# Performance work log

Measured on AMD Instinct MI355X. Metric: run time of the kernel, lower is better.

## Reference

```python
import jax, jax.numpy as jnp
import numpy as np

D = 1024           # input_size
D2 = 2 * D         # hidden width of the three inner linears
OUT = 1024         # output_size
S = 8192           # tokens per example


def setup_inputs() -> dict:
    key = jax.random.key(0)
    ks = jax.random.split(key, 11)
    def lin(k, fan_in, fan_out):
        bound = 1.0 / np.sqrt(fan_in)
        kw, kb = jax.random.split(k)
        W = jax.random.uniform(kw, (fan_in, fan_out), jnp.float32, -bound, bound)
        b = jax.random.uniform(kb, (fan_out,), jnp.float32, -bound, bound)
        return W, b
    W_in, b_in = lin(ks[0], D, D2)      # reading_example_input
    W_out, b_out = lin(ks[1], D, D2)    # reading_example_output
    W_cat, b_cat = lin(ks[2], D2, D2)   # concatenated_layer_map
    W_fin, b_fin = lin(ks[3], D2, OUT)  # final_map
    return {
        "input_embedding": jax.random.normal(ks[4], (1, S, D), jnp.float32),
        "output_embedding": jax.random.normal(ks[5], (1, S, D), jnp.float32),
        "random_augmentation": jax.random.normal(ks[6], (1, S, D), jnp.float32),
        "W_in": W_in, "b_in": b_in,
        "W_out": W_out, "b_out": b_out,
        "W_cat": W_cat, "b_cat": b_cat,
        "W_fin": W_fin, "b_fin": b_fin,
    }


def reference(input_embedding, output_embedding, random_augmentation,
              W_in, b_in, W_out, b_out, W_cat, b_cat, W_fin, b_fin):
    def march(x, y):
        # x, y: [1, S, D]
        iq = jax.nn.softmax(x @ W_in + b_in, axis=-1)[0]    # [S, 2D]
        oq = jax.nn.softmax(y @ W_out + b_out, axis=-1)[0]  # [S, 2D]
        cat = jnp.concatenate((x, y), axis=-1)[0]           # [S, 2D]
        icm = jax.nn.softmax(cat @ W_cat + b_cat, axis=-1)  # [S, 2D]
        iqk = iq.T @ icm                                    # [2D, 2D]
        oqk = oq.T @ icm                                    # [2D, 2D]
        meta = jax.nn.relu(iqk @ oqk.T)                     # [2D, 2D]
        scale = jnp.sqrt(jnp.float32(icm.shape[-1]))
        res = (icm @ meta) / scale                          # [S, 2D]
        return jax.nn.relu(res @ W_fin + b_fin)             # [S, OUT]

    transformation = march(input_embedding, output_embedding)
    random_desc = march(input_embedding, random_augmentation)
    return (transformation, random_desc)
```

## Files before the change

### kernel.cpp

```cpp
#include <hip/hip_runtime.h>

#define S_TOK 8192
#define DIM   1024
#define DIM2  2048
#define OUTN  1024

typedef __bf16 bf16x8 __attribute__((ext_vector_type(8)));
typedef float  f32x4  __attribute__((ext_vector_type(4)));
typedef short  s16x8  __attribute__((ext_vector_type(8)));
typedef unsigned short u16x4 __attribute__((ext_vector_type(4)));

__device__ __forceinline__ unsigned short f2bf(float x) {
  unsigned u = __builtin_bit_cast(unsigned, x);
  u = (u + 0x7FFFu + ((u >> 16) & 1u)) >> 16;
  return (unsigned short)u;
}
__device__ __forceinline__ float bf2f(unsigned short u) {
  return __builtin_bit_cast(float, (unsigned)u << 16);
}

__device__ __forceinline__ void gld_lds16(const void* g, void* l) {
  auto* g1 = reinterpret_cast<__attribute__((address_space(1))) unsigned*>(
      (unsigned long long)g);
  auto* l3 = reinterpret_cast<__attribute__((address_space(3))) unsigned*>(
      (unsigned long long)l);
  __builtin_amdgcn_global_load_lds(g1, l3, 16, 0, 0);
}

__device__ __forceinline__ int lds_off(int idx, int k) {
  int b = (idx << 7) + (k << 1);
  b ^= ((idx ^ (idx >> 3)) & 7) << 4;
  return b;
}

struct PrepTab {
  const float* in[3]; unsigned short* out[3];
  const float* win[4]; unsigned short* wout[4]; int R[4]; int C[4];
};
__global__ __launch_bounds__(256) void prep_all(PrepTab t) {
  __shared__ unsigned short tl[64 * 64];
  const int tid = threadIdx.x;
  if (blockIdx.z < 3) {
    const float* in = t.in[blockIdx.z];
    unsigned short* out = t.out[blockIdx.z];
    int i = blockIdx.x * 256 + tid;
    float4 v = ((const float4*)in)[i];
    u16x4 o;
    o[0] = f2bf(v.x); o[1] = f2bf(v.y); o[2] = f2bf(v.z); o[3] = f2bf(v.w);
    *(u16x4*)(out + (size_t)i * 4) = o;
    return;
  }
  int x = blockIdx.x;
  if (x >= 4096) return;
  int wz = x >> 10, rem = x & 1023, bx = rem & 31, by = rem >> 5;
  const int R = t.R[wz], C = t.C[wz];
  const int r0 = by << 6, c0 = bx << 6;
  if (r0 >= R || c0 >= C) return;
  const float* in = t.win[wz];
  unsigned short* out = t.wout[wz];
#pragma unroll
  for (int i = 0; i < 2; ++i) {
    int ch = tid + (i << 8);
    int r = ch >> 3, c8 = (ch & 7) << 3;
    const float* p = in + (size_t)(r0 + r) * C + c0 + c8;
    float4 a = *(const float4*)p, b = *(const float4*)(p + 4);
    s16x8 w;
    w[0] = (short)f2bf(a.x); w[1] = (short)f2bf(a.y);
    w[2] = (short)f2bf(a.z); w[3] = (short)f2bf(a.w);
    w[4] = (short)f2bf(b.x); w[5] = (short)f2bf(b.y);
    w[6] = (short)f2bf(b.z); w[7] = (short)f2bf(b.w);
    int sw = ((r ^ (r >> 3)) & 7) << 3;
    *(s16x8*)&tl[(r << 6) + (c8 ^ sw)] = w;
  }
  __syncthreads();
#pragma unroll
  for (int i = 0; i < 2; ++i) {
    int ch = tid + (i << 8);
    int c = ch >> 3, r8 = (ch & 7) << 3;
    s16x8 w;
#pragma unroll
    for (int j = 0; j < 8; ++j) {
      int rr = r8 + j;
      w[j] = (short)tl[(rr << 6) + (c ^ (((rr ^ (rr >> 3)) & 7) << 3))];
    }
    *(s16x8*)(out + (size_t)(c0 + c) * R + r0 + r8) = w;
  }
}

struct SmTab { unsigned short* T[6]; };
__global__ __launch_bounds__(512) void softmax_cols(SmTab tab) {
  unsigned short* T = tab.T[blockIdx.y];
  const int tid = threadIdx.x;
  const int colg = tid & 63, seg = tid >> 6;
  const size_t c = ((size_t)blockIdx.x << 6) + colg;
  float m = -1e30f, s = 0.f;
  for (int n = seg; n < DIM2; n += 8) {
    float v = bf2f(T[(size_t)n * S_TOK + c]);
    float mn = fmaxf(m, v);
    s = s * __expf(m - mn) + __expf(v - mn);
    m = mn;
  }
  __shared__ float redm[512], reds[512];
  redm[tid] = m; reds[tid] = s;
  __syncthreads();
  if (seg == 0) {
    float M = m, S = s;
#pragma unroll
    for (int k = 1; k < 8; ++k) {
      float mk = redm[colg + (k << 6)], sk = reds[colg + (k << 6)];
      float mn = fmaxf(M, mk);
      S = S * __expf(M - mn) + sk * __expf(mk - mn);
      M = mn;
    }
    redm[colg] = M; reds[colg] = 1.0f / S;
  }
  __syncthreads();
  m = redm[colg];
  const float inv = reds[colg];
  for (int n = seg; n < DIM2; n += 8) {
    size_t idx = (size_t)n * S_TOK + c;
    T[idx] = f2bf(__expf(bf2f(T[idx]) - m) * inv);
  }
}

struct GPtr {
  const unsigned short* A[6];
  const unsigned short* Arow2[6];
  const unsigned short* B[6];
  const unsigned short* Bk2[6];
  const float* bias[6];
  void* C[6];
  int Ks[6];
  int ldas[6];
};
struct TPar { const unsigned short* src[2]; unsigned short* dst[2]; };

template <int BIAS_ROW, int OUT_BF16, int NZG>
__global__ __launch_bounds__(256, 3) void gemm_nt(GPtr p, TPar tp, int ldb, int ldc,
                                                  float scale, int do_relu) {
  __shared__ __align__(16) char lds[32768];
  const int z = blockIdx.z;
  const int tid  = threadIdx.x;

  if (NZG >= 0 && z >= NZG) {
    const unsigned short* src = tp.src[z - NZG];
    unsigned short* dst = tp.dst[z - NZG];
    unsigned short* tl = (unsigned short*)lds;
    const int nblk = gridDim.x * gridDim.y;
    int bid = blockIdx.y * gridDim.x + blockIdx.x;
    for (int it = bid; it < (DIM2 / 64) * (S_TOK / 64); it += nblk) {
      int tx = it & (S_TOK / 64 - 1), ty = it >> 7;
      int r0 = ty << 6, c0 = tx << 6;
#pragma unroll
      for (int i = 0; i < 2; ++i) {
        int ch = tid + (i << 8);
        int r = ch >> 3, c8 = (ch & 7) << 3;
        s16x8 w = *(const s16x8*)(src + (size_t)(r0 + r) * S_TOK + c0 + c8);
        int sw = ((r ^ (r >> 3)) & 7) << 3;
        *(s16x8*)&tl[(r << 6) + (c8 ^ sw)] = w;
      }
      __syncthreads();
#pragma unroll
      for (int i = 0; i < 2; ++i) {
        int ch = tid + (i << 8);
        int c = ch >> 3, r8 = (ch & 7) << 3;
        s16x8 w;
#pragma unroll
        for (int j = 0; j < 8; ++j) {
          int rr = r8 + j;
          w[j] = (short)tl[(rr << 6) + (c ^ (((rr ^ (rr >> 3)) & 7) << 3))];
        }
        *(s16x8*)(dst + (size_t)(c0 + c) * DIM2 + r0 + r8) = w;
      }
      __syncthreads();
    }
    return;
  }

  char* As = lds;
  char* Bs = lds + 16384;
  const int lane = tid & 63;
  const int wave = tid >> 6;
  const int wm = (wave >> 1) << 6;
  const int wn = (wave & 1) << 6;
  const int m0 = blockIdx.y << 7;
  const int n0 = blockIdx.x << 7;
  const int lda = p.ldas[z];
  const int K = p.Ks[z];

  const unsigned short* Au = p.A[z];
  const unsigned short* B  = p.B[z];
  const float* bias = p.bias[z];
  void* Cv = p.C[z];

  int srow[4], sgk[4];
#pragma unroll
  for (int i = 0; i < 4; ++i) {
    int c = (wave << 8) + (i << 6) + lane;
    int row = c >> 3, kc = c & 7;
    srow[i] = row;
    sgk[i]  = (kc ^ ((row ^ (row >> 3)) & 7)) << 3;
  }

  f32x4 acc[4][4];
#pragma unroll
  for (int i = 0; i < 4; ++i)
#pragma unroll
    for (int j = 0; j < 4; ++j) acc[i][j] = {0.f, 0.f, 0.f, 0.f};

  for (int k0 = 0; k0 < K; k0 += 64) {
#pragma unroll
    for (int i = 0; i < 4; ++i) {
      char* dA = As + (((wave << 2) + i) << 10);
      char* dB = Bs + (((wave << 2) + i) << 10);
      gld_lds16(Au + (size_t)(m0 + srow[i]) * lda + k0 + sgk[i], dA);
      gld_lds16(B  + (size_t)(n0 + srow[i]) * ldb + k0 + sgk[i], dB);
    }
    __syncthreads();
#pragma unroll
    for (int ks = 0; ks < 2; ++ks) {
      bf16x8 af[4], bfr[4];
      int kk = (ks << 5) + ((lane >> 4) << 3);
#pragma unroll
      for (int t = 0; t < 4; ++t) {
        af[t]  = *(const bf16x8*)(As + lds_off(wm + (t << 4) + (lane & 15), kk));
        bfr[t] = *(const bf16x8*)(Bs + lds_off(wn + (t << 4) + (lane & 15), kk));
      }
#pragma unroll
      for (int mt = 0; mt < 4; ++mt)
#pragma unroll
        for (int nt = 0; nt < 4; ++nt)
          acc[mt][nt] = __builtin_amdgcn_mfma_f32_16x16x32_bf16(af[mt], bfr[nt], acc[mt][nt], 0, 0, 0);
    }
    __syncthreads();
  }

  if (OUT_BF16) {
    unsigned short* ct = (unsigned short*)lds;
    __syncthreads();
#pragma unroll
    for (int nt = 0; nt < 4; ++nt) {
      int cl = wn + (nt << 4) + (lane & 15);
      float bcol = (!BIAS_ROW && bias) ? bias[n0 + cl] : 0.0f;
#pragma unroll
      for (int mt = 0; mt < 4; ++mt) {
#pragma unroll
        for (int r = 0; r < 4; ++r) {
          int rl = wm + (mt << 4) + ((lane >> 4) << 2) + r;
          float bv = BIAS_ROW ? (bias ? bias[m0 + rl] : 0.0f) : bcol;
          float v = acc[mt][nt][r] * scale + bv;
          if (do_relu) v = fmaxf(v, 0.0f);
          ct[(rl << 7) + (cl ^ (((rl >> 2) & 3) << 4))] = f2bf(v);
        }
      }
    }
    __syncthreads();
#pragma unroll
    for (int it = 0; it < 8; ++it) {
      int c = (it << 8) + tid;
      int rl = c >> 4, co = (c & 15) << 3;
      s16x8 w = *(const s16x8*)(ct + (rl << 7) + (co ^ (((rl >> 2) & 3) << 4)));
      *(s16x8*)((unsigned short*)Cv + (size_t)(m0 + rl) * ldc + n0 + co) = w;
    }
  } else {
#pragma unroll
    for (int nt = 0; nt < 4; ++nt) {
      int col = n0 + wn + (nt << 4) + (lane & 15);
      float bcol = (!BIAS_ROW && bias) ? bias[col] : 0.0f;
#pragma unroll
      for (int mt = 0; mt < 4; ++mt) {
        f32x4 a = acc[mt][nt];
#pragma unroll
        for (int r = 0; r < 4; ++r) {
          int rowg = m0 + wm + (mt << 4) + ((lane >> 4) << 2) + r;
          float bv = BIAS_ROW ? (bias ? bias[rowg] : 0.0f) : bcol;
          float v = a[r] * scale + bv;
          if (do_relu) v = fmaxf(v, 0.0f);
          ((float*)Cv)[(size_t)rowg * ldc + col] = v;
        }
      }
    }
  }
}

template <int ASPLIT, int BSPLIT, int BIAS_ROW, int OUT_BF16, int PHASES>
__global__ __launch_bounds__(512, 2) void gemm256(GPtr p, int ldb, int ldc,
                                                  float scale, int do_relu,
                                                  int RW, int XW) {
  __shared__ __align__(16) char lds[131072];
  const int z = blockIdx.z;
  const int tid  = threadIdx.x;
  const int lane = tid & 63;
  const int wave = tid >> 6;
  const int wm   = wave >> 2;
  const int wn   = wave & 3;
  const int lda  = p.ldas[z];
  const int K    = p.Ks[z];

  const int gx = gridDim.x;
  const int nper = (gx * gridDim.y) >> 3;
  const int RH = nper / RW;
  int bid = blockIdx.y * gx + blockIdx.x;
  int xcd = bid & 7, j = bid >> 3;
  const int n0 = (RW * (xcd % XW) + (j % RW)) << 8;
  const int m0 = (RH * (xcd / XW) + (j / RW)) << 8;

  const unsigned short* Au = p.A[z];
  int mb = m0;
  if (ASPLIT && m0 >= 2048) { Au = p.Arow2[z]; mb = m0 - 2048; }
  const unsigned short* Bp = p.B[z];
  const float* bias = p.bias[z];
  void* Cv = p.C[z];

  const int NT = K >> 6;

  int srow_[2], skel_[2];
#pragma unroll
  for (int i = 0; i < 2; ++i) {
    int row = (i << 7) + (wave << 4) + (lane >> 2);
    srow_[i] = row;
    skel_[i] = ((lane & 3) ^ ((row >> 1) & 3)) << 3;
  }
  const unsigned short* aB[2];
  const unsigned short* bB[2];
  const unsigned short* b2B[2];
#pragma unroll
  for (int i = 0; i < 2; ++i) {
    aB[i]  = Au + (size_t)(mb + srow_[i]) * lda + skel_[i];
    bB[i]  = Bp + (size_t)(n0 + srow_[i]) * ldb + skel_[i];
    b2B[i] = BSPLIT ? (p.Bk2[z] + (size_t)(n0 + srow_[i]) * ldb + skel_[i] - DIM)
                    : bB[i];
  }

  auto stage_unit = [&](int t, int u) {
    const int k0 = t << 6;
    const int h  = u >> 1;
    char* base = lds + ((t & 1) << 16) + ((u & 1) << 15) + (h << 14) + (wave << 10);
#pragma unroll
    for (int i = 0; i < 2; ++i) {
      const unsigned short* src;
      if (u & 1) src = ((BSPLIT && k0 >= DIM) ? b2B[i] : bB[i]) + k0 + (h << 5);
      else       src = aB[i] + k0 + (h << 5);
      gld_lds16(src, base + (i << 13));
    }
  };

  auto rdA = [&](const char* buf, int h, int mf) -> bf16x8 {
    int row = (wm << 7) + (mf << 4) + (lane & 15);
    int col = (lane >> 4) ^ ((row >> 1) & 3);
    return *(const bf16x8*)(buf + (h << 14) + (row << 6) + (col << 4));
  };
  auto rdB = [&](const char* buf, int h, int nf) -> bf16x8 {
    int row = (wn << 6) + (nf << 4) + (lane & 15);
    int col = (lane >> 4) ^ ((row >> 1) & 3);
    return *(const bf16x8*)(buf + 32768 + (h << 14) + (row << 6) + (col << 4));
  };

  f32x4 acc[8][4];
#pragma unroll
  for (int i = 0; i < 8; ++i)
#pragma unroll
    for (int j2 = 0; j2 < 4; ++j2) acc[i][j2] = {0.f, 0.f, 0.f, 0.f};

  stage_unit(0, 0); stage_unit(0, 1); stage_unit(0, 2); stage_unit(0, 3);

  for (int t = 0; t < NT; ++t) {
    const char* buf = lds + ((t & 1) << 16);
    const bool more = (t + 1 < NT);

    if (PHASES == 2) {
      bf16x8 aq[8], bq[4];
      if (more) {
        stage_unit(t + 1, 0); stage_unit(t + 1, 1);
        asm volatile("s_waitcnt vmcnt(8)" ::: "memory");
      } else {
        asm volatile("s_waitcnt vmcnt(4)" ::: "memory");
      }
      __builtin_amdgcn_s_barrier();
      __builtin_amdgcn_sched_barrier(0);
#pragma unroll
      for (int nf = 0; nf < 4; ++nf) bq[nf] = rdB(buf, 0, nf);
#pragma unroll
      for (int mf = 0; mf < 8; ++mf) aq[mf] = rdA(buf, 0, mf);
      __builtin_amdgcn_s_setprio(1);
#pragma unroll
      for (int mf = 0; mf < 8; ++mf)
#pragma unroll
        for (int nf = 0; nf < 4; ++nf)
          acc[mf][nf] = __builtin_amdgcn_mfma_f32_16x16x32_bf16(aq[mf], bq[nf], acc[mf][nf], 0, 0, 0);
      __builtin_amdgcn_s_setprio(0);
      __builtin_amdgcn_s_barrier();
      if (more) {
        stage_unit(t + 1, 2); stage_unit(t + 1, 3);
        asm volatile("s_waitcnt vmcnt(8)" ::: "memory");
      } else {
        asm volatile("s_waitcnt vmcnt(0)" ::: "memory");
      }
      __builtin_amdgcn_s_barrier();
      __builtin_amdgcn_sched_barrier(0);
#pragma unroll
      for (int nf = 0; nf < 4; ++nf) bq[nf] = rdB(buf, 1, nf);
#pragma unroll
      for (int mf = 0; mf < 8; ++mf) aq[mf] = rdA(buf, 1, mf);
      __builtin_amdgcn_s_setprio(1);
#pragma unroll
      for (int mf = 0; mf < 8; ++mf)
#pragma unroll
        for (int nf = 0; nf < 4; ++nf)
          acc[mf][nf] = __builtin_amdgcn_mfma_f32_16x16x32_bf16(aq[mf], bq[nf], acc[mf][nf], 0, 0, 0);
      __builtin_amdgcn_s_setprio(0);
      __builtin_amdgcn_s_barrier();
    } else {
      bf16x8 aq[4], bq[4];
      if (more) { stage_unit(t + 1, 0); asm volatile("s_waitcnt vmcnt(6)" ::: "memory"); }
      else      { asm volatile("s_waitcnt vmcnt(4)" ::: "memory"); }
      __builtin_amdgcn_s_barrier();
      __builtin_amdgcn_sched_barrier(0);
#pragma unroll
      for (int nf = 0; nf < 4; ++nf) bq[nf] = rdB(buf, 0, nf);
#pragma unroll
      for (int mf = 0; mf < 4; ++mf) aq[mf] = rdA(buf, 0, mf);
      __builtin_amdgcn_s_setprio(1);
#pragma unroll
      for (int mf = 0; mf < 4; ++mf)
#pragma unroll
        for (int nf = 0; nf < 4; ++nf)
          acc[mf][nf] = __builtin_amdgcn_mfma_f32_16x16x32_bf16(aq[mf], bq[nf], acc[mf][nf], 0, 0, 0);
      __builtin_amdgcn_s_setprio(0);
      __builtin_amdgcn_s_barrier();
#pragma unroll
      for (int mf = 0; mf < 4; ++mf) aq[mf] = rdA(buf, 0, mf + 4);
      if (more) stage_unit(t + 1, 1);
      __builtin_amdgcn_s_setprio(1);
#pragma unroll
      for (int mf = 0; mf < 4; ++mf)
#pragma unroll
        for (int nf = 0; nf < 4; ++nf)
          acc[mf + 4][nf] = __builtin_amdgcn_mfma_f32_16x16x32_bf16(aq[mf], bq[nf], acc[mf + 4][nf], 0, 0, 0);
      __builtin_amdgcn_s_setprio(0);
      __builtin_amdgcn_s_barrier();
      if (more) { stage_unit(t + 1, 2); asm volatile("s_waitcnt vmcnt(6)" ::: "memory"); }
      else      { asm volatile("s_waitcnt vmcnt(0)" ::: "memory"); }
      __builtin_amdgcn_s_barrier();
      __builtin_amdgcn_sched_barrier(0);
#pragma unroll
      for (int nf = 0; nf < 4; ++nf) bq[nf] = rdB(buf, 1, nf);
#pragma unroll
      for (int mf = 0; mf < 4; ++mf) aq[mf] = rdA(buf, 1, mf);
      __builtin_amdgcn_s_setprio(1);
#pragma unroll
      for (int mf = 0; mf < 4; ++mf)
#pragma unroll
        for (int nf = 0; nf < 4; ++nf)
          acc[mf][nf] = __builtin_amdgcn_mfma_f32_16x16x32_bf16(aq[mf], bq[nf], acc[mf][nf], 0, 0, 0);
      __builtin_amdgcn_s_setprio(0);
      __builtin_amdgcn_s_barrier();
#pragma unroll
      for (int mf = 0; mf < 4; ++mf) aq[mf] = rdA(buf, 1, mf + 4);
      if (more) stage_unit(t + 1, 3);
      __builtin_amdgcn_s_setprio(1);
#pragma unroll
      for (int mf = 0; mf < 4; ++mf)
#pragma unroll
        for (int nf = 0; nf < 4; ++nf)
          acc[mf + 4][nf] = __builtin_amdgcn_mfma_f32_16x16x32_bf16(aq[mf], bq[nf], acc[mf + 4][nf], 0, 0, 0);
      __builtin_amdgcn_s_setprio(0);
      __builtin_amdgcn_s_barrier();
    }
  }

  __syncthreads();
  if (OUT_BF16) {
    unsigned short* ct = (unsigned short*)lds;
#pragma unroll
    for (int nf = 0; nf < 4; ++nf) {
      int cl = (wn << 6) + (nf << 4) + (lane & 15);
      float bcol = (!BIAS_ROW && bias) ? bias[n0 + cl] : 0.0f;
#pragma unroll
      for (int mf = 0; mf < 8; ++mf) {
#pragma unroll
        for (int r = 0; r < 4; ++r) {
          int rl = (wm << 7) + (mf << 4) + ((lane >> 4) << 2) + r;
          float bv = BIAS_ROW ? (bias ? bias[m0 + rl] : 0.0f) : bcol;
          float v = acc[mf][nf][r] * scale + bv;
          if (do_relu) v = fmaxf(v, 0.0f);
          ct[(rl << 8) + (cl ^ (((rl >> 2) & 3) << 4))] = f2bf(v);
        }
      }
    }
    __syncthreads();
#pragma unroll
    for (int it = 0; it < 16; ++it) {
      int c = (it << 9) + tid;
      int rl = c >> 5, co = (c & 31) << 3;
      s16x8 w = *(const s16x8*)(ct + (rl << 8) + (co ^ (((rl >> 2) & 3) << 4)));
      *(s16x8*)((unsigned short*)Cv + (size_t)(m0 + rl) * ldc + n0 + co) = w;
    }
  } else {
    float* ctf = (float*)lds;
#pragma unroll
    for (int h = 0; h < 2; ++h) {
      if (h) __syncthreads();
      if (wm == h) {
#pragma unroll
        for (int nf = 0; nf < 4; ++nf) {
          int cl = (wn << 6) + (nf << 4) + (lane & 15);
          float bcol = (!BIAS_ROW && bias) ? bias[n0 + cl] : 0.0f;
#pragma unroll
          for (int mf = 0; mf < 8; ++mf) {
#pragma unroll
            for (int r = 0; r < 4; ++r) {
              int rl2 = (mf << 4) + ((lane >> 4) << 2) + r;
              float bv = BIAS_ROW ? (bias ? bias[m0 + (h << 7) + rl2] : 0.0f) : bcol;
              float v = acc[mf][nf][r] * scale + bv;
              if (do_relu) v = fmaxf(v, 0.0f);
              ctf[(rl2 << 8) + (cl ^ (((rl2 >> 2) & 3) << 3))] = v;
            }
          }
        }
      }
      __syncthreads();
#pragma unroll
      for (int it = 0; it < 16; ++it) {
        int c = (it << 9) + tid;
        int rl2 = c >> 6, co = (c & 63) << 2;
        float4 w = *(const float4*)(ctf + (rl2 << 8) + (co ^ (((rl2 >> 2) & 3) << 3)));
        *(float4*)((float*)Cv + (size_t)(m0 + (h << 7) + rl2) * ldc + n0 + co) = w;
      }
    }
  }
}

extern "C" void kernel_launch(void* const* d_in, const int* in_sizes, int n_in,
                              void* d_out, int out_size, void* d_ws, size_t ws_size,
                              hipStream_t stream) {
  const float* X   = (const float*)d_in[0];
  const float* Y   = (const float*)d_in[1];
  const float* R   = (const float*)d_in[2];
  const float* Wi  = (const float*)d_in[3];
  const float* bi  = (const float*)d_in[4];
  const float* Wo  = (const float*)d_in[5];
  const float* bo  = (const float*)d_in[6];
  const float* Wc  = (const float*)d_in[7];
  const float* bc  = (const float*)d_in[8];
  const float* Wf  = (const float*)d_in[9];
  const float* bf_ = (const float*)d_in[10];
  float* out = (float*)d_out;

  char* ws = (char*)d_ws;
  size_t off = 0;
  auto alloc = [&](size_t b) { char* p = ws + off; off += (b + 255) & ~(size_t)255; return p; };
  unsigned short* Xb   = (unsigned short*)alloc((size_t)S_TOK * DIM  * 2);
  unsigned short* Yb   = (unsigned short*)alloc((size_t)S_TOK * DIM  * 2);
  unsigned short* Rb   = (unsigned short*)alloc((size_t)S_TOK * DIM  * 2);
  unsigned short* WiT  = (unsigned short*)alloc((size_t)DIM2 * DIM  * 2);
  unsigned short* WoT  = (unsigned short*)alloc((size_t)DIM2 * DIM  * 2);
  unsigned short* WcT  = (unsigned short*)alloc((size_t)DIM2 * DIM2 * 2);
  unsigned short* WfT  = (unsigned short*)alloc((size_t)OUTN * DIM2 * 2);
  unsigned short* iqT  = (unsigned short*)alloc((size_t)DIM2 * S_TOK * 2);
  unsigned short* oqT0 = (unsigned short*)alloc((size_t)DIM2 * S_TOK * 2);
  unsigned short* oqT1 = (unsigned short*)alloc((size_t)DIM2 * S_TOK * 2);
  unsigned short* icmT0= (unsigned short*)alloc((size_t)DIM2 * S_TOK * 2);
  unsigned short* icmT1= (unsigned short*)alloc((size_t)DIM2 * S_TOK * 2);
  unsigned short* iqk0 = Xb;
  unsigned short* oqk0 = Xb + (size_t)DIM2*DIM2;
  unsigned short* iqk1 = Yb;
  unsigned short* oqk1 = Yb + (size_t)DIM2*DIM2;
  unsigned short* meta0= iqT;
  unsigned short* meta1= iqT + (size_t)DIM2*DIM2;
  unsigned short* MWT0 = iqT + (size_t)2*DIM2*DIM2;
  unsigned short* MWT1 = iqT + (size_t)2*DIM2*DIM2 + (size_t)OUTN*DIM2;
  unsigned short* icm0 = oqT0;
  unsigned short* icm1 = oqT1;

  {
    PrepTab t{};
    t.in[0] = X; t.in[1] = Y; t.in[2] = R;
    t.out[0] = Xb; t.out[1] = Yb; t.out[2] = Rb;
    t.win[0] = Wi; t.wout[0] = WiT; t.R[0] = DIM;  t.C[0] = DIM2;
    t.win[1] = Wo; t.wout[1] = WoT; t.R[1] = DIM;  t.C[1] = DIM2;
    t.win[2] = Wc; t.wout[2] = WcT; t.R[2] = DIM2; t.C[2] = DIM2;
    t.win[3] = Wf; t.wout[3] = WfT; t.R[3] = DIM2; t.C[3] = OUTN;
    prep_all<<<dim3((S_TOK * DIM / 4) / 256, 1, 4), 256, 0, stream>>>(t);
  }

  const float rscale = 0.022097086912079608f;

  {
    GPtr g{};
    g.A[0] = WcT; g.B[0] = Xb; g.Bk2[0] = Yb; g.bias[0] = bc; g.C[0] = icmT0;
    g.Ks[0] = DIM2; g.ldas[0] = DIM2;
    g.A[1] = WcT; g.B[1] = Xb; g.Bk2[1] = Rb; g.bias[1] = bc; g.C[1] = icmT1;
    g.Ks[1] = DIM2; g.ldas[1] = DIM2;
    g.A[2] = WiT; g.B[2] = Xb; g.Bk2[2] = Xb; g.bias[2] = bi; g.C[2] = iqT;
    g.Ks[2] = DIM; g.ldas[2] = DIM;
    g.A[3] = WoT; g.B[3] = Yb; g.Bk2[3] = Yb; g.bias[3] = bo; g.C[3] = oqT0;
    g.Ks[3] = DIM; g.ldas[3] = DIM;
    g.A[4] = WoT; g.B[4] = Rb; g.Bk2[4] = Rb; g.bias[4] = bo; g.C[4] = oqT1;
    g.Ks[4] = DIM; g.ldas[4] = DIM;
    gemm256<0,1,1,1,2><<<dim3(S_TOK/256, DIM2/256, 5), 512, 0, stream>>>(
        g, DIM, S_TOK, 1.f, 0, 4, 8);
  }
  {
    SmTab st{};
    st.T[0] = iqT; st.T[1] = oqT0; st.T[2] = oqT1; st.T[3] = icmT0; st.T[4] = icmT1;
    softmax_cols<<<dim3(S_TOK / 64, 5), dim3(512), 0, stream>>>(st);
  }
  {
    GPtr g{};
    g.A[0] = iqT; g.A[1] = iqT;
    g.Arow2[0] = oqT0; g.Arow2[1] = oqT1;
    g.B[0] = icmT0; g.B[1] = icmT1;
    g.C[0] = iqk0; g.C[1] = iqk1;
    g.Ks[0] = S_TOK; g.Ks[1] = S_TOK;
    g.ldas[0] = S_TOK; g.ldas[1] = S_TOK;
    gemm256<1,0,0,1,4><<<dim3(DIM2/256, 4096/256, 2), 512, 0, stream>>>(
        g, S_TOK, DIM2, 1.f, 0, 4, 2);
  }
  {
    GPtr g{};
    g.A[0] = iqk0; g.B[0] = oqk0; g.C[0] = meta0; g.Ks[0] = DIM2; g.ldas[0] = DIM2;
    g.A[1] = iqk1; g.B[1] = oqk1; g.C[1] = meta1; g.Ks[1] = DIM2; g.ldas[1] = DIM2;
    TPar tp{};
    tp.src[0] = icmT0; tp.dst[0] = icm0;
    tp.src[1] = icmT1; tp.dst[1] = icm1;
    gemm_nt<0,1,2><<<dim3(DIM2/128, DIM2/128, 4), 256, 0, stream>>>(
        g, tp, DIM2, DIM2, 1.f, 1);
  }
  {
    GPtr g{};
    g.A[0] = WfT; g.B[0] = meta0; g.C[0] = MWT0; g.Ks[0] = DIM2; g.ldas[0] = DIM2;
    g.A[1] = WfT; g.B[1] = meta1; g.C[1] = MWT1; g.Ks[1] = DIM2; g.ldas[1] = DIM2;
    TPar tp{};
    gemm_nt<0,1,2><<<dim3(DIM2/128, OUTN/128, 2), 256, 0, stream>>>(
        g, tp, DIM2, DIM2, rscale, 0);
  }
  {
    GPtr g{};
    g.A[0] = icm0; g.B[0] = MWT0; g.bias[0] = bf_; g.C[0] = out;
    g.Ks[0] = DIM2; g.ldas[0] = DIM2;
    g.A[1] = icm1; g.B[1] = MWT1; g.bias[1] = bf_;
    g.C[1] = out + (size_t)S_TOK * OUTN;
    g.Ks[1] = DIM2; g.ldas[1] = DIM2;
    gemm256<0,0,0,0,4><<<dim3(OUTN/256, S_TOK/256, 2), 512, 0, stream>>>(
        g, DIM2, OUTN, 1.f, 1, 4, 1);
  }
  (void)in_sizes; (void)n_in; (void)out_size; (void)ws_size;
}
```

Before: 872.3 us.

## Share the X-half of the concat projection across both marches

The concatenated-layer GEMM is split into its X and Y/R halves of W_cat. The X half is computed once, in the same launch as the input-query projection, with the biases packed into a combined vector. It is then copied to the second march's buffer, and a second launch adds each march's Y or R contribution through a read-add in the bf16 epilogue. This drops one of the two redundant X·W_cat computations. In exchange it adds a 32 MB device copy, an extra launch, a read-modify-write of the output, and an additional bf16 rounding of the logits before softmax.

New measurement: 901.5 us. 3.3% more time.

```diff
diff --git a/kernel.cpp b/kernel.cpp
--- a/kernel.cpp
+++ b/kernel.cpp
@@ -36,6 +36,8 @@
 struct PrepTab {
   const float* in[3]; unsigned short* out[3];
   const float* win[4]; unsigned short* wout[4]; int R[4]; int C[4];
+  const float* bi; const float* bc; const float* bo;
+  float* sbX; float* sbY;
 };
 __global__ __launch_bounds__(256) void prep_all(PrepTab t) {
   __shared__ unsigned short tl[64 * 64];
@@ -51,7 +53,14 @@
     return;
   }
   int x = blockIdx.x;
-  if (x >= 4096) return;
+  if (x >= 4096) {
+    if (x < 4112) {
+      int idx = ((x - 4096) << 8) + tid;
+      t.sbX[idx] = (idx < 2048) ? t.bi[idx] : t.bc[idx - 2048];
+      t.sbY[idx] = (idx < 2048) ? t.bo[idx] : 0.0f;
+    }
+    return;
+  }
   int wz = x >> 10, rem = x & 1023, bx = rem & 31, by = rem >> 5;
   const int R = t.R[wz], C = t.C[wz];
   const int r0 = by << 6, c0 = bx << 6;
@@ -130,6 +139,7 @@
   const unsigned short* Bk2[6];
   const float* bias[6];
   void* C[6];
+  void* C2[6];
   int Ks[6];
   int ldas[6];
 };
@@ -283,10 +293,10 @@
   }
 }
 
-template <int ASPLIT, int BSPLIT, int BIAS_ROW, int OUT_BF16, int PHASES>
+template <int ASPLIT, int BSPLIT, int BIAS_ROW, int OUT_BF16, int PHASES, int CADD>
 __global__ __launch_bounds__(512, 2) void gemm256(GPtr p, int ldb, int ldc,
                                                   float scale, int do_relu,
-                                                  int RW, int XW) {
+                                                  int RW, int XW, int lda2) {
   __shared__ __align__(16) char lds[131072];
   const int z = blockIdx.z;
   const int tid  = threadIdx.x;
@@ -294,7 +304,6 @@
   const int wave = tid >> 6;
   const int wm   = wave >> 2;
   const int wn   = wave & 3;
-  const int lda  = p.ldas[z];
   const int K    = p.Ks[z];
 
   const int gx = gridDim.x;
@@ -305,12 +314,14 @@
   const int n0 = (RW * (xcd % XW) + (j % RW)) << 8;
   const int m0 = (RH * (xcd / XW) + (j / RW)) << 8;
 
-  const unsigned short* Au = p.A[z];
-  int mb = m0;
-  if (ASPLIT && m0 >= 2048) { Au = p.Arow2[z]; mb = m0 - 2048; }
+  const bool upper = ASPLIT && (m0 >= 2048);
+  const unsigned short* Au = upper ? p.Arow2[z] : p.A[z];
+  const int mb  = upper ? m0 - 2048 : m0;
+  const int lda = upper ? lda2 : p.ldas[z];
   const unsigned short* Bp = p.B[z];
   const float* bias = p.bias[z];
-  void* Cv = p.C[z];
+  void* Cv = upper ? p.C2[z] : p.C[z];
+  const int mo = upper ? m0 - 2048 : m0;
 
   const int NT = K >> 6;
 
@@ -494,7 +505,15 @@
       int c = (it << 9) + tid;
       int rl = c >> 5, co = (c & 31) << 3;
       s16x8 w = *(const s16x8*)(ct + (rl << 8) + (co ^ (((rl >> 2) & 3) << 4)));
-      *(s16x8*)((unsigned short*)Cv + (size_t)(m0 + rl) * ldc + n0 + co) = w;
+      unsigned short* dst = (unsigned short*)Cv + (size_t)(mo + rl) * ldc + n0 + co;
+      if (CADD && upper) {
+        s16x8 old = *(const s16x8*)dst;
+#pragma unroll
+        for (int jj = 0; jj < 8; ++jj)
+          w[jj] = (short)f2bf(bf2f((unsigned short)w[jj]) +
+                              bf2f((unsigned short)old[jj]));
+      }
+      *(s16x8*)dst = w;
     }
   } else {
     float* ctf = (float*)lds;
@@ -525,7 +544,7 @@
         int c = (it << 9) + tid;
         int rl2 = c >> 6, co = (c & 63) << 2;
         float4 w = *(const float4*)(ctf + (rl2 << 8) + (co ^ (((rl2 >> 2) & 3) << 3)));
-        *(float4*)((float*)Cv + (size_t)(m0 + (h << 7) + rl2) * ldc + n0 + co) = w;
+        *(float4*)((float*)Cv + (size_t)(mo + (h << 7) + rl2) * ldc + n0 + co) = w;
       }
     }
   }
@@ -557,6 +576,8 @@
   unsigned short* WoT  = (unsigned short*)alloc((size_t)DIM2 * DIM  * 2);
   unsigned short* WcT  = (unsigned short*)alloc((size_t)DIM2 * DIM2 * 2);
   unsigned short* WfT  = (unsigned short*)alloc((size_t)OUTN * DIM2 * 2);
+  float* sbX = (float*)alloc(4096 * 4);
+  float* sbY = (float*)alloc(4096 * 4);
   unsigned short* iqT  = (unsigned short*)alloc((size_t)DIM2 * S_TOK * 2);
   unsigned short* oqT0 = (unsigned short*)alloc((size_t)DIM2 * S_TOK * 2);
   unsigned short* oqT1 = (unsigned short*)alloc((size_t)DIM2 * S_TOK * 2);
@@ -581,6 +602,7 @@
     t.win[1] = Wo; t.wout[1] = WoT; t.R[1] = DIM;  t.C[1] = DIM2;
     t.win[2] = Wc; t.wout[2] = WcT; t.R[2] = DIM2; t.C[2] = DIM2;
     t.win[3] = Wf; t.wout[3] = WfT; t.R[3] = DIM2; t.C[3] = OUTN;
+    t.bi = bi; t.bc = bc; t.bo = bo; t.sbX = sbX; t.sbY = sbY;
     prep_all<<<dim3((S_TOK * DIM / 4) / 256, 1, 4), 256, 0, stream>>>(t);
   }
 
@@ -588,18 +610,24 @@
 
   {
     GPtr g{};
-    g.A[0] = WcT; g.B[0] = Xb; g.Bk2[0] = Yb; g.bias[0] = bc; g.C[0] = icmT0;
-    g.Ks[0] = DIM2; g.ldas[0] = DIM2;
-    g.A[1] = WcT; g.B[1] = Xb; g.Bk2[1] = Rb; g.bias[1] = bc; g.C[1] = icmT1;
-    g.Ks[1] = DIM2; g.ldas[1] = DIM2;
-    g.A[2] = WiT; g.B[2] = Xb; g.Bk2[2] = Xb; g.bias[2] = bi; g.C[2] = iqT;
-    g.Ks[2] = DIM; g.ldas[2] = DIM;
-    g.A[3] = WoT; g.B[3] = Yb; g.Bk2[3] = Yb; g.bias[3] = bo; g.C[3] = oqT0;
-    g.Ks[3] = DIM; g.ldas[3] = DIM;
-    g.A[4] = WoT; g.B[4] = Rb; g.Bk2[4] = Rb; g.bias[4] = bo; g.C[4] = oqT1;
-    g.Ks[4] = DIM; g.ldas[4] = DIM;
-    gemm256<0,1,1,1,2><<<dim3(S_TOK/256, DIM2/256, 5), 512, 0, stream>>>(
-        g, DIM, S_TOK, 1.f, 0, 4, 8);
+    g.A[0] = WiT;  g.Arow2[0] = WcT;  g.B[0] = Xb;
+    g.bias[0] = sbX; g.C[0] = iqT; g.C2[0] = icmT0;
+    g.Ks[0] = DIM; g.ldas[0] = DIM;
+    gemm256<1,0,1,1,2,0><<<dim3(S_TOK/256, 4096/256, 1), 512, 0, stream>>>(
+        g, DIM, S_TOK, 1.f, 0, 8, 4, DIM2);
+  }
+  hipMemcpyAsync(icmT1, icmT0, (size_t)DIM2 * S_TOK * 2,
+                 hipMemcpyDeviceToDevice, stream);
+  {
+    GPtr g{};
+    g.A[0] = WoT; g.Arow2[0] = WcT + 1024; g.B[0] = Yb;
+    g.bias[0] = sbY; g.C[0] = oqT0; g.C2[0] = icmT0;
+    g.Ks[0] = DIM; g.ldas[0] = DIM;
+    g.A[1] = WoT; g.Arow2[1] = WcT + 1024; g.B[1] = Rb;
+    g.bias[1] = sbY; g.C[1] = oqT1; g.C2[1] = icmT1;
+    g.Ks[1] = DIM; g.ldas[1] = DIM;
+    gemm256<1,0,1,1,2,1><<<dim3(S_TOK/256, 4096/256, 2), 512, 0, stream>>>(
+        g, DIM, S_TOK, 1.f, 0, 8, 4, DIM2);
   }
   {
     SmTab st{};
@@ -612,10 +640,11 @@
     g.Arow2[0] = oqT0; g.Arow2[1] = oqT1;
     g.B[0] = icmT0; g.B[1] = icmT1;
     g.C[0] = iqk0; g.C[1] = iqk1;
+    g.C2[0] = oqk0; g.C2[1] = oqk1;
     g.Ks[0] = S_TOK; g.Ks[1] = S_TOK;
     g.ldas[0] = S_TOK; g.ldas[1] = S_TOK;
-    gemm256<1,0,0,1,4><<<dim3(DIM2/256, 4096/256, 2), 512, 0, stream>>>(
-        g, S_TOK, DIM2, 1.f, 0, 4, 2);
+    gemm256<1,0,0,1,4,0><<<dim3(DIM2/256, 4096/256, 2), 512, 0, stream>>>(
+        g, S_TOK, DIM2, 1.f, 0, 4, 2, S_TOK);
   }
   {
     GPtr g{};
@@ -642,8 +671,8 @@
     g.A[1] = icm1; g.B[1] = MWT1; g.bias[1] = bf_;
     g.C[1] = out + (size_t)S_TOK * OUTN;
     g.Ks[1] = DIM2; g.ldas[1] = DIM2;
-    gemm256<0,0,0,0,4><<<dim3(OUTN/256, S_TOK/256, 2), 512, 0, stream>>>(
-        g, DIM2, OUTN, 1.f, 1, 4, 1);
+    gemm256<0,0,0,0,4,0><<<dim3(OUTN/256, S_TOK/256, 2), 512, 0, stream>>>(
+        g, DIM2, OUTN, 1.f, 1, 4, 1, DIM2);
   }
   (void)in_sizes; (void)n_in; (void)out_size; (void)ws_size;
 }
```
